# Kernel optimization log

Hardware: AMD Instinct MI355X
Metric: run time of the kernel (lower is better)

## Reference

```python
import jax, jax.numpy as jnp
import numpy as np

B, T, S = 32, 200, 256          # batch, decoder steps, encoder (memory) length
L = 512                          # latent_dims
U = 2 * L                        # LSTM units / attention units / attention_layer_size
E = 512                          # encoder memory feature dim
M = 80                           # mel_bins


def setup_inputs() -> dict:
    key = jax.random.key(0)
    ks = jax.random.split(key, 16)
    s = 0.05
    inputs = jax.random.normal(ks[0], (B, T, M), jnp.float32)
    memory = jax.random.normal(ks[1], (B, S, E), jnp.float32)
    # pre-net: Dense(2L, relu) -> Dropout -> Dense(L, relu) -> Dropout
    W1 = jax.random.normal(ks[2], (M, 2 * L), jnp.float32) * s
    b1 = jnp.zeros((2 * L,), jnp.float32)
    W2 = jax.random.normal(ks[3], (2 * L, L), jnp.float32) * s
    b2 = jnp.zeros((L,), jnp.float32)
    # LSTMCell(2L): input = concat(prenet_out [L], attention [U=2L]) -> 3L
    Wx = jax.random.normal(ks[4], (3 * L, 4 * U), jnp.float32) * s
    Wh = jax.random.normal(ks[5], (U, 4 * U), jnp.float32) * s
    b_lstm = jnp.zeros((4 * U,), jnp.float32)
    # Bahdanau attention (units=U): memory_layer, query_layer (no bias), score vector v
    Wm = jax.random.normal(ks[6], (E, U), jnp.float32) * s
    Wq = jax.random.normal(ks[7], (U, U), jnp.float32) * s
    v_att = jax.random.normal(ks[8], (U,), jnp.float32) * s
    # attention_layer (Dense, no bias): concat(cell_output [U], context [E]) -> U
    Wa = jax.random.normal(ks[9], (U + E, U), jnp.float32) * s
    # output projection to mel bins
    Wp = jax.random.normal(ks[10], (U, M), jnp.float32) * s
    bp = jnp.zeros((M,), jnp.float32)
    return dict(inputs=inputs, memory=memory, W1=W1, b1=b1, W2=W2, b2=b2,
                Wx=Wx, Wh=Wh, b_lstm=b_lstm, Wm=Wm, Wq=Wq, v_att=v_att,
                Wa=Wa, Wp=Wp, bp=bp)


def reference(inputs, memory, W1, b1, W2, b2, Wx, Wh, b_lstm, Wm, Wq, v_att, Wa, Wp, bp):
    # pre-net (inference: dropout is identity)
    x = jax.nn.relu(inputs @ W1 + b1)
    x = jax.nn.relu(x @ W2 + b2)                       # [B,T,L]
    keys = memory @ Wm                                 # precomputed attention keys [B,S,U]

    def step(carry, xt):
        h, c, attn = carry
        cell_in = jnp.concatenate([xt, attn], axis=-1)  # [B, 3L]
        z = cell_in @ Wx + h @ Wh + b_lstm              # [B, 4U]
        i, f, g, o = jnp.split(z, 4, axis=-1)
        c_new = jax.nn.sigmoid(f) * c + jax.nn.sigmoid(i) * jnp.tanh(g)
        h_new = jax.nn.sigmoid(o) * jnp.tanh(c_new)
        # Bahdanau additive attention
        q = h_new @ Wq                                  # [B,U]
        score = jnp.einsum('u,bsu->bs', v_att, jnp.tanh(keys + q[:, None, :]))
        align = jax.nn.softmax(score, axis=-1)          # [B,S]
        ctx = jnp.einsum('bs,bse->be', align, memory)   # [B,E]
        attn_new = jnp.concatenate([h_new, ctx], axis=-1) @ Wa  # [B,U]
        return (h_new, c_new, attn_new), attn_new

    init = (jnp.zeros((B, U), x.dtype), jnp.zeros((B, U), x.dtype), jnp.zeros((B, U), x.dtype))
    xs = jnp.swapaxes(x, 0, 1)                          # [T,B,L]
    (h, c, attn), ys = jax.lax.scan(step, init, xs)
    outs = jnp.swapaxes(ys, 0, 1)                       # [B,T,U]
    mel = outs @ Wp + bp                                # [B,T,M]
    return (mel, h, c, attn)
```

## Files before the change

kernel.cpp:

```cpp
#include <hip/hip_runtime.h>


typedef unsigned short us16;
typedef unsigned int u32;
typedef unsigned long long u64;
typedef __attribute__((ext_vector_type(8))) short bf16x8;
typedef __attribute__((ext_vector_type(4))) float f32x4;

#define MFMA16 __builtin_amdgcn_mfma_f32_16x16x32_bf16
#define AGT __HIP_MEMORY_SCOPE_AGENT

__device__ __forceinline__ us16 f2bf(float f){
  u32 u = __builtin_bit_cast(u32, f);
  u += 0x7fffu + ((u >> 16) & 1u);
  return (us16)(u >> 16);
}
__device__ __forceinline__ float bf2f(us16 h){
  return __builtin_bit_cast(float, ((u32)h) << 16);
}
__device__ __forceinline__ float h2f(us16 u){
  _Float16 h = __builtin_bit_cast(_Float16, u); return (float)h;
}
__device__ __forceinline__ us16 f2h(float f){
  _Float16 h = (_Float16)f; return __builtin_bit_cast(us16, h);
}
__device__ __forceinline__ void split3(float v, us16& s0, us16& s1, us16& s2){
  s0 = f2bf(v); float r = v - bf2f(s0);
  s1 = f2bf(r); r -= bf2f(s1);
  s2 = f2bf(r);
}
__device__ __forceinline__ float tanh_fast(float x){
  float e = __expf(-2.f * fmaxf(x, -40.f));
  return (1.f - e) / (1.f + e);
}

__device__ __forceinline__ u32 aload32(const u32* p){
  return __hip_atomic_load(p, __ATOMIC_RELAXED, AGT);
}
__device__ __forceinline__ void astoref(float* p, float v){
  __hip_atomic_store(p, v, __ATOMIC_RELAXED, AGT);
}
__device__ __forceinline__ void aaddf(float* p, float v){
  __hip_atomic_fetch_add(p, v, __ATOMIC_RELAXED, AGT);
}
__device__ __forceinline__ bf16x8 pin_reg(bf16x8 v){
  f32x4 t = __builtin_bit_cast(f32x4, v);
  asm volatile("" : "+v"(t));
  return __builtin_bit_cast(bf16x8, t);
}
__device__ __forceinline__ void f32_frag3(const float* p, float rs,
                                          bf16x8& f0, bf16x8& f1, bf16x8& f2){
  float4 t0 = *(const float4*)p;
  float4 t1 = *(const float4*)(p + 4);
  float tf[8] = {t0.x, t0.y, t0.z, t0.w, t1.x, t1.y, t1.z, t1.w};
#pragma unroll
  for (int i = 0; i < 8; ++i){
    float v = tf[i] * rs;
    us16 s0, s1, s2; split3(v, s0, s1, s2);
    f0[i] = (short)s0; f1[i] = (short)s1; f2[i] = (short)s2;
  }
}

#define OFF_WTA    0ull
#define OFF_WQT    50331648ull
#define OFF_X2P    56623104ull
#define OFF_KEYH   76283904ull
#define OFF_KEYL   93061120ull
#define OFF_X1     76283904ull
#define OFF_HIST   109838336ull
#define OFF_HROLL  129597440ull
#define OFF_UCROLL 155942912ull
#define OFF_SROLL  169115648ull
#define OFF_QROLL  169141376ull
#define OFF_CBUF   195355776ull
#define OFF_WAPN   195486848ull
#define OFF_BPERM  195732608ull
#define OFF_BAR    195748992ull
#define TOTAL_WS   195750016ull

#define WTPL 8388608ull
#define WQPL 1048576ull
#define X2PL 3276800ull

__global__ void k_zero_init(float* hroll0, float* ucroll, float* sroll,
                            float* cbuf, u32* bar){
  u32 id = blockIdx.x * 256u + threadIdx.x;
  const u32 gs = 65536u;
  for (u32 i = id; i < 32768u;   i += gs) hroll0[i] = 0.f;
  for (u32 i = id; i < 3293184u; i += gs) ucroll[i] = 0.f;
  for (u32 i = id; i < 6432u;    i += gs) sroll[i]  = (i < 32u) ? 1.f : 0.f;
  for (u32 i = id; i < 32768u;   i += gs) cbuf[i]   = 0.f;
  for (u32 i = id; i < 256u;     i += gs) bar[i]    = 0u;
}

__global__ void k_bperm(const float* __restrict__ bl, float* __restrict__ bpm){
  int c = blockIdx.x * 256 + threadIdx.x;
  if (c < 4096) bpm[((c & 1023) << 2) | (c >> 10)] = bl[c];
}

__global__ void k_transp3(const float* __restrict__ src, us16* __restrict__ dst,
                          int srows, int scols, int ldd, long long pstride, int perm){
  __shared__ float tile[32][33];
  int bx = blockIdx.x * 32, by = blockIdx.y * 32;
  int tx = threadIdx.x & 31, ty = threadIdx.x >> 5;
#pragma unroll
  for (int i = 0; i < 4; ++i){
    int r = by + ty + i * 8, c = bx + tx;
    tile[ty + i * 8][tx] = (r < srows && c < scols) ? src[(size_t)r * scols + c] : 0.f;
  }
  __syncthreads();
#pragma unroll
  for (int i = 0; i < 4; ++i){
    int c = bx + ty + i * 8;
    int r = by + tx;
    if (c < scols && r < srows){
      int oc = perm ? (((c & 1023) << 2) | (c >> 10)) : c;
      float v = tile[tx][ty + i * 8];
      us16 s0, s1, s2; split3(v, s0, s1, s2);
      size_t base = (size_t)oc * ldd + r;
      dst[base] = s0; dst[(size_t)pstride + base] = s1; dst[2ull * pstride + base] = s2;
    }
  }
}

template<int NP, int AF, int BF>
__global__ void __launch_bounds__(256)
k_gemm3(const void* __restrict__ Ap, const void* __restrict__ Bp, void* __restrict__ outp,
        int M, int N, int K, int mode, const float* __restrict__ aux, int ldd){
  __shared__ us16 At[NP][128][72];
  __shared__ us16 Bt[NP][64][72];
  const int tid = threadIdx.x, wv = tid >> 6, lane = tid & 63;
  const int r0 = lane & 15, kg = lane >> 4;
  const int rb = blockIdx.x * 128, cb = blockIdx.y * 64;
  f32x4 acc[2][4];
#pragma unroll
  for (int a = 0; a < 2; ++a)
#pragma unroll
    for (int b = 0; b < 4; ++b) acc[a][b] = (f32x4){0.f, 0.f, 0.f, 0.f};

  const int nkt = (K + 63) >> 6;
  for (int kt = 0; kt < nkt; ++kt){
    const int kb = kt * 64;
    for (int e = tid; e < 8192; e += 256){
      int r = e >> 6, k = e & 63, ga = rb + r, gk = kb + k;
      bool ok = (ga < M) && (gk < K);
      if constexpr (AF){
        float v = ok ? ((const float*)Ap)[(size_t)ga * K + gk] : 0.f;
        us16 s0, s1, s2; split3(v, s0, s1, s2);
        At[0][r][k] = s0;
        if constexpr (NP == 3){ At[1][r][k] = s1; At[2][r][k] = s2; }
      } else {
        At[0][r][k] = ok ? ((const us16*)Ap)[(size_t)ga * K + gk] : (us16)0;
      }
    }
    for (int e = tid; e < 4096; e += 256){
      int kr = e >> 6, c = e & 63, gk = kb + kr, gc = cb + c;
      bool ok = (gk < K) && (gc < N);
      if constexpr (BF){
        float v = ok ? ((const float*)Bp)[(size_t)gk * N + gc] : 0.f;
        us16 s0, s1, s2; split3(v, s0, s1, s2);
        Bt[0][c][kr] = s0;
        if constexpr (NP == 3){ Bt[1][c][kr] = s1; Bt[2][c][kr] = s2; }
      } else {
        Bt[0][c][kr] = ok ? ((const us16*)Bp)[(size_t)gk * N + gc] : (us16)0;
      }
    }
    __syncthreads();
#pragma unroll
    for (int kk = 0; kk < 64; kk += 32){
      bf16x8 af[NP][2];
#pragma unroll
      for (int p = 0; p < NP; ++p){
        af[p][0] = *(const bf16x8*)&At[p][wv * 32 + r0][kk + kg * 8];
        af[p][1] = *(const bf16x8*)&At[p][wv * 32 + 16 + r0][kk + kg * 8];
      }
#pragma unroll
      for (int cf = 0; cf < 4; ++cf){
        bf16x8 bv[NP];
#pragma unroll
        for (int p = 0; p < NP; ++p) bv[p] = *(const bf16x8*)&Bt[p][cf * 16 + r0][kk + kg * 8];
#pragma unroll
        for (int rf = 0; rf < 2; ++rf){
          acc[rf][cf] = MFMA16(af[0][rf], bv[0], acc[rf][cf], 0, 0, 0);
          if constexpr (NP == 3){
            acc[rf][cf] = MFMA16(af[0][rf], bv[1], acc[rf][cf], 0, 0, 0);
            acc[rf][cf] = MFMA16(af[1][rf], bv[0], acc[rf][cf], 0, 0, 0);
            acc[rf][cf] = MFMA16(af[0][rf], bv[2], acc[rf][cf], 0, 0, 0);
            acc[rf][cf] = MFMA16(af[1][rf], bv[1], acc[rf][cf], 0, 0, 0);
            acc[rf][cf] = MFMA16(af[2][rf], bv[0], acc[rf][cf], 0, 0, 0);
          }
        }
      }
    }
    __syncthreads();
  }
  us16* o16 = (us16*)outp; float* of = (float*)outp;
#pragma unroll
  for (int rf = 0; rf < 2; ++rf)
#pragma unroll
    for (int cf = 0; cf < 4; ++cf)
#pragma unroll
      for (int i = 0; i < 4; ++i){
        int r = rb + wv * 32 + rf * 16 + kg * 4 + i;
        int c = cb + cf * 16 + r0;
        if (r >= M || c >= N) continue;
        float v = acc[rf][cf][i];
        if (mode == 0){
          of[(size_t)r * ldd + c] = fmaxf(v + aux[c], 0.f);
        } else if (mode == 1){
          v = fmaxf(v + aux[c], 0.f);
          us16 s0, s1, s2; split3(v, s0, s1, s2);
          size_t b2 = (size_t)r * ldd + c;
          o16[b2] = s0; o16[X2PL + b2] = s1; o16[2 * X2PL + b2] = s2;
        } else if (mode == 2){
          us16 hh = f2h(v); float rem = v - h2f(hh); us16 hl = f2h(rem);
          size_t b2 = (size_t)r * 1024 + c;
          o16[b2] = hh; o16[WTPL + b2] = hl;
        } else if (mode == 3){
          float w = v + (r < 1024 ? aux[(size_t)r * 4096 + c] : 0.f);
          int pc = (c & 1023) * 4 + (c >> 10);
          us16 s0, s1, s2; split3(w, s0, s1, s2);
          size_t b2 = (size_t)pc * 2048 + 512 + r;
          o16[b2] = s0; o16[WTPL + b2] = s1; o16[2 * WTPL + b2] = s2;
        } else if (mode == 4){
          o16[(size_t)r * ldd + c] = f2bf(v);
        } else if (mode == 5){
          of[((size_t)(r & 31) * 200 + (r >> 5)) * 80 + c] = v + aux[c];
        } else {
          of[(size_t)r * ldd + c] = v;
        }
      }
}

__device__ __forceinline__ void gbar(u32* bar, u32 ep, int tid, int blk){
  __syncthreads();
  if (tid == 0){
    asm volatile("s_waitcnt vmcnt(0)" ::: "memory");
    u32 g = (u32)(blk >> 5);
    u32 old = __hip_atomic_fetch_add(&bar[g * 32], 1u, __ATOMIC_RELAXED, AGT);
    if (old == 32u * ep - 1u){
      u32 r = __hip_atomic_fetch_add(&bar[248], 1u, __ATOMIC_RELAXED, AGT);
      if (r == 8u * ep - 1u)
        __hip_atomic_store(&bar[252], ep, __ATOMIC_RELAXED, AGT);
    }
    while (aload32(&bar[252]) < ep) __builtin_amdgcn_s_sleep(1);
    __builtin_amdgcn_sched_barrier(0);
  }
  __syncthreads();
}

struct CoopA {
  const us16 *wta, *wqt, *x2p, *kh, *kl;
  const float *mem, *vatt, *bperm;
  us16 *hist;
  float *hroll, *ucroll, *sroll, *qroll, *cbuf;
  u32 *bar;
};

__global__ void __launch_bounds__(512, 2) k_coop(CoopA a){
  __shared__ us16 khi[32][1024];
  __shared__ us16 klo[32][1024];
  __shared__ float zp[8][512];
  __shared__ float esc[32];
  __shared__ float rs_lds[32];

  __builtin_amdgcn_fence(__ATOMIC_ACQUIRE, "agent");

  const int tid = threadIdx.x, blk = blockIdx.x;
  const int wv = tid >> 6, lane = tid & 63;
  const int r0 = lane & 15, kg = lane >> 4;
  const int cb_b = blk >> 3, cb_s0 = (blk & 7) * 32;
  const int colbase = blk * 16;
  const int u0 = lane * 16;

  bf16x8 wr[8][3];
#pragma unroll
  for (int ks = 0; ks < 8; ++ks){
    const size_t wb = (size_t)(colbase + r0) * 2048 + (size_t)wv * 256 + ks * 32 + kg * 8;
#pragma unroll
    for (int p = 0; p < 3; ++p)
      wr[ks][p] = pin_reg(*(const bf16x8*)&a.wta[(size_t)p * WTPL + wb]);
  }
  bf16x8 wq[4][3];
  if (blk < 64){
#pragma unroll
    for (int ks = 0; ks < 4; ++ks){
      const size_t wb = (size_t)(colbase + r0) * 1024 + (size_t)wv * 128 + ks * 32 + kg * 8;
#pragma unroll
      for (int p = 0; p < 3; ++p)
        wq[ks][p] = pin_reg(*(const bf16x8*)&a.wqt[(size_t)p * WQPL + wb]);
    }
  }

  {
    const size_t kbase = ((size_t)(cb_b * 256 + cb_s0)) * 1024;
    for (int i = tid; i < 4096; i += 512){
      int r = i >> 7, c8 = (i & 127) * 8;
      *(bf16x8*)&khi[r][c8] = *(const bf16x8*)&a.kh[kbase + (size_t)r * 1024 + c8];
      *(bf16x8*)&klo[r][c8] = *(const bf16x8*)&a.kl[kbase + (size_t)r * 1024 + c8];
    }
  }
  __syncthreads();

  u32 ep = 0;
  for (int t = 0; t < 200; ++t){
    {
      if (tid < 32) rs_lds[tid] = 1.f / a.sroll[(size_t)t * 32 + tid];
      __syncthreads();
      if (tid < 64){
        int flat = blk * 64 + tid;
        int b = flat >> 9, e = flat & 511;
        float v = a.ucroll[(size_t)t * 16384 + flat];
        a.hist[(size_t)(t * 32 + b) * 1536 + 1024 + e] = f2bf(v * rs_lds[b]);
      }
      f32x4 acc0 = (f32x4){0.f,0.f,0.f,0.f}, acc1 = acc0;
#pragma unroll
      for (int ks = 0; ks < 8; ++ks){
        const int k0 = wv * 256 + ks * 32;
        const int kf = k0 + kg * 8;
        bf16x8 w0 = wr[ks][0], w1 = wr[ks][1], w2 = wr[ks][2];
        bf16x8 a00, a01, a02, a10, a11, a12;
        if (wv < 2){
          const size_t xb0 = ((size_t)r0 * 200 + t) * 512 + kf;
          const size_t xb1 = ((size_t)(r0 + 16) * 200 + t) * 512 + kf;
          a00 = *(const bf16x8*)&a.x2p[xb0];
          a01 = *(const bf16x8*)&a.x2p[X2PL + xb0];
          a02 = *(const bf16x8*)&a.x2p[2 * X2PL + xb0];
          a10 = *(const bf16x8*)&a.x2p[xb1];
          a11 = *(const bf16x8*)&a.x2p[X2PL + xb1];
          a12 = *(const bf16x8*)&a.x2p[2 * X2PL + xb1];
        } else if (wv < 6){
          const int hk = kf - 512;
          const float* hp0 = a.hroll + (size_t)t * 32768 + (size_t)r0 * 1024 + hk;
          f32_frag3(hp0,         1.f, a00, a01, a02);
          f32_frag3(hp0 + 16384, 1.f, a10, a11, a12);
        } else {
          const int ek = kf - 1536;
          const float* up = a.ucroll + (size_t)t * 16384 + (size_t)r0 * 512 + ek;
          f32_frag3(up,        rs_lds[r0],      a00, a01, a02);
          f32_frag3(up + 8192, rs_lds[r0 + 16], a10, a11, a12);
        }
        acc0 = MFMA16(a00, w0, acc0, 0,0,0); acc0 = MFMA16(a00, w1, acc0, 0,0,0);
        acc0 = MFMA16(a01, w0, acc0, 0,0,0); acc0 = MFMA16(a00, w2, acc0, 0,0,0);
        acc0 = MFMA16(a01, w1, acc0, 0,0,0); acc0 = MFMA16(a02, w0, acc0, 0,0,0);
        acc1 = MFMA16(a10, w0, acc1, 0,0,0); acc1 = MFMA16(a10, w1, acc1, 0,0,0);
        acc1 = MFMA16(a11, w0, acc1, 0,0,0); acc1 = MFMA16(a10, w2, acc1, 0,0,0);
        acc1 = MFMA16(a11, w1, acc1, 0,0,0); acc1 = MFMA16(a12, w0, acc1, 0,0,0);
      }
#pragma unroll
      for (int i = 0; i < 4; ++i){
        zp[wv][(kg * 4 + i) * 16 + r0]      = acc0[i];
        zp[wv][(16 + kg * 4 + i) * 16 + r0] = acc1[i];
      }
      __syncthreads();
      float z = 0.f;
#pragma unroll
      for (int w = 0; w < 8; ++w) z += zp[w][tid];
      z += a.bperm[colbase + (tid & 15)];
      __syncthreads();
      zp[0][tid] = z;
      __syncthreads();
      if (tid < 128){
        int b = tid >> 2, ul = tid & 3, u = blk * 4 + ul;
        float zi = zp[0][b * 16 + ul * 4 + 0];
        float zf = zp[0][b * 16 + ul * 4 + 1];
        float zg = zp[0][b * 16 + ul * 4 + 2];
        float zo = zp[0][b * 16 + ul * 4 + 3];
        float co = a.cbuf[b * 1024 + u];
        float cn = (1.f / (1.f + expf(-zf))) * co + (1.f / (1.f + expf(-zi))) * tanhf(zg);
        float hn = (1.f / (1.f + expf(-zo))) * tanhf(cn);
        a.cbuf[b * 1024 + u] = cn;
        astoref(&a.hroll[(size_t)(t + 1) * 32768 + b * 1024 + u], hn);
        us16 s0, s1, s2; split3(hn, s0, s1, s2);
        a.hist[((size_t)(t + 1) * 32 + b) * 1536 + u] = s0;
      }
    }
    gbar(a.bar, ++ep, tid, blk);

    if (blk < 64){
      f32x4 acc0 = (f32x4){0.f,0.f,0.f,0.f}, acc1 = acc0;
#pragma unroll
      for (int ks = 0; ks < 4; ++ks){
        const int kf = wv * 128 + ks * 32 + kg * 8;
        bf16x8 w0 = wq[ks][0], w1 = wq[ks][1], w2 = wq[ks][2];
        bf16x8 a00, a01, a02, a10, a11, a12;
        const float* hp0 = a.hroll + (size_t)(t + 1) * 32768 + (size_t)r0 * 1024 + kf;
        f32_frag3(hp0,         1.f, a00, a01, a02);
        f32_frag3(hp0 + 16384, 1.f, a10, a11, a12);
        acc0 = MFMA16(a00, w0, acc0, 0,0,0); acc0 = MFMA16(a00, w1, acc0, 0,0,0);
        acc0 = MFMA16(a01, w0, acc0, 0,0,0); acc0 = MFMA16(a00, w2, acc0, 0,0,0);
        acc0 = MFMA16(a01, w1, acc0, 0,0,0); acc0 = MFMA16(a02, w0, acc0, 0,0,0);
        acc1 = MFMA16(a10, w0, acc1, 0,0,0); acc1 = MFMA16(a10, w1, acc1, 0,0,0);
        acc1 = MFMA16(a11, w0, acc1, 0,0,0); acc1 = MFMA16(a10, w2, acc1, 0,0,0);
        acc1 = MFMA16(a11, w1, acc1, 0,0,0); acc1 = MFMA16(a12, w0, acc1, 0,0,0);
      }
#pragma unroll
      for (int i = 0; i < 4; ++i){
        zp[wv][(kg * 4 + i) * 16 + r0]      = acc0[i];
        zp[wv][(16 + kg * 4 + i) * 16 + r0] = acc1[i];
      }
      __syncthreads();
      float q = 0.f;
#pragma unroll
      for (int w = 0; w < 8; ++w) q += zp[w][tid];
      astoref(&a.qroll[(size_t)t * 32768 + (size_t)(tid >> 4) * 1024 + colbase + (tid & 15)], q);
    }
    gbar(a.bar, ++ep, tid, blk);

    {
      float qv[16], vv[16];
      {
        const float* qp = a.qroll + (size_t)t * 32768 + (size_t)cb_b * 1024 + u0;
        float4 q0 = *(const float4*)qp;
        float4 q1 = *(const float4*)(qp + 4);
        float4 q2 = *(const float4*)(qp + 8);
        float4 q3 = *(const float4*)(qp + 12);
        qv[0]=q0.x; qv[1]=q0.y; qv[2]=q0.z; qv[3]=q0.w;
        qv[4]=q1.x; qv[5]=q1.y; qv[6]=q1.z; qv[7]=q1.w;
        qv[8]=q2.x; qv[9]=q2.y; qv[10]=q2.z; qv[11]=q2.w;
        qv[12]=q3.x; qv[13]=q3.y; qv[14]=q3.z; qv[15]=q3.w;
        float4 v0 = *(const float4*)(a.vatt + u0);
        float4 v1 = *(const float4*)(a.vatt + u0 + 4);
        float4 v2 = *(const float4*)(a.vatt + u0 + 8);
        float4 v3 = *(const float4*)(a.vatt + u0 + 12);
        vv[0]=v0.x; vv[1]=v0.y; vv[2]=v0.z; vv[3]=v0.w;
        vv[4]=v1.x; vv[5]=v1.y; vv[6]=v1.z; vv[7]=v1.w;
        vv[8]=v2.x; vv[9]=v2.y; vv[10]=v2.z; vv[11]=v2.w;
        vv[12]=v3.x; vv[13]=v3.y; vv[14]=v3.z; vv[15]=v3.w;
      }
#pragma unroll
      for (int m = 0; m < 4; ++m){
        const int sl = wv * 4 + m;
        bf16x8 h0 = *(const bf16x8*)&khi[sl][u0];
        bf16x8 h1 = *(const bf16x8*)&khi[sl][u0 + 8];
        bf16x8 l0 = *(const bf16x8*)&klo[sl][u0];
        bf16x8 l1 = *(const bf16x8*)&klo[sl][u0 + 8];
        float part = 0.f;
#pragma unroll
        for (int j = 0; j < 8; ++j){
          float kva = h2f((us16)h0[j]) + h2f((us16)l0[j]);
          part += vv[j] * tanh_fast(kva + qv[j]);
          float kvb = h2f((us16)h1[j]) + h2f((us16)l1[j]);
          part += vv[8 + j] * tanh_fast(kvb + qv[8 + j]);
        }
#pragma unroll
        for (int off = 32; off; off >>= 1) part += __shfl_xor(part, off);
        if (lane == 0) esc[sl] = __expf(part);
      }
      __syncthreads();
      if (tid == 0){
        float bs = 0.f;
#pragma unroll
        for (int i = 0; i < 32; ++i) bs += esc[i];
        aaddf(&a.sroll[(size_t)(t + 1) * 32 + cb_b], bs);
      }
      {
        float ac0 = 0.f, ac1 = 0.f, ac2 = 0.f, ac3 = 0.f;
        const float* mrow = a.mem + ((size_t)(cb_b * 256 + cb_s0)) * 512 + tid;
#pragma unroll
        for (int j = 0; j < 32; j += 4){
          ac0 += esc[j]     * mrow[(size_t)j * 512];
          ac1 += esc[j + 1] * mrow[(size_t)(j + 1) * 512];
          ac2 += esc[j + 2] * mrow[(size_t)(j + 2) * 512];
          ac3 += esc[j + 3] * mrow[(size_t)(j + 3) * 512];
        }
        aaddf(&a.ucroll[(size_t)(t + 1) * 16384 + cb_b * 512 + tid], (ac0 + ac1) + (ac2 + ac3));
      }
    }
    gbar(a.bar, ++ep, tid, blk);
  }

  {
    if (tid < 32) rs_lds[tid] = 1.f / a.sroll[(size_t)200 * 32 + tid];
    __syncthreads();
    if (tid < 64){
      int flat = blk * 64 + tid;
      int b = flat >> 9, e = flat & 511;
      float v = a.ucroll[(size_t)200 * 16384 + flat];
      a.hist[(size_t)(200 * 32 + b) * 1536 + 1024 + e] = f2bf(v * rs_lds[b]);
    }
  }
}

__global__ void k_copy_hc(const float* __restrict__ h, const float* __restrict__ c,
                          float* __restrict__ out){
  int i = blockIdx.x * 256 + threadIdx.x;
  if (i < 32768){
    out[512000 + i] = h[i];
    out[544768 + i] = c[i];
  }
}

extern "C" void kernel_launch(void* const* d_in, const int* in_sizes, int n_in,
                              void* d_out, int out_size, void* d_ws, size_t ws_size,
                              hipStream_t stream){
  const float* inputs = (const float*)d_in[0];
  const float* memory = (const float*)d_in[1];
  const float* W1     = (const float*)d_in[2];
  const float* b1     = (const float*)d_in[3];
  const float* W2     = (const float*)d_in[4];
  const float* b2     = (const float*)d_in[5];
  const float* Wx     = (const float*)d_in[6];
  const float* Wh     = (const float*)d_in[7];
  const float* b_lstm = (const float*)d_in[8];
  const float* Wm     = (const float*)d_in[9];
  const float* Wq     = (const float*)d_in[10];
  const float* v_att  = (const float*)d_in[11];
  const float* Wa     = (const float*)d_in[12];
  const float* Wp     = (const float*)d_in[13];
  const float* bp     = (const float*)d_in[14];
  float* out = (float*)d_out;
  char* ws = (char*)d_ws;
  if (ws_size < TOTAL_WS) return;

  us16* WTA    = (us16*)(ws + OFF_WTA);
  us16* WQT    = (us16*)(ws + OFF_WQT);
  us16* X2P    = (us16*)(ws + OFF_X2P);
  us16* KEYH   = (us16*)(ws + OFF_KEYH);
  float* X1    = (float*)(ws + OFF_X1);
  us16* HIST   = (us16*)(ws + OFF_HIST);
  float* HROLL = (float*)(ws + OFF_HROLL);
  float* UCROLL= (float*)(ws + OFF_UCROLL);
  float* SROLL = (float*)(ws + OFF_SROLL);
  float* QROLL = (float*)(ws + OFF_QROLL);
  float* CBUF  = (float*)(ws + OFF_CBUF);
  us16* WAPN   = (us16*)(ws + OFF_WAPN);
  float* BPM   = (float*)(ws + OFF_BPERM);
  u32*  BAR    = (u32*)(ws + OFF_BAR);

  k_zero_init<<<256, 256, 0, stream>>>(HROLL, UCROLL, SROLL, CBUF, BAR);
  k_bperm<<<16, 256, 0, stream>>>(b_lstm, BPM);
  k_transp3<<<dim3(32, 32), 256, 0, stream>>>(Wq, WQT, 1024, 1024, 1024, (long long)WQPL, 0);
  k_transp3<<<dim3(128, 16), 256, 0, stream>>>(Wx, WTA, 512, 4096, 2048, (long long)WTPL, 1);

  k_gemm3<3,1,1><<<dim3(12, 64), 256, 0, stream>>>(Wa, Wx + (size_t)512 * 4096, WTA,
                                                   1536, 4096, 1024, 3, Wh, 0);
  k_gemm3<3,1,1><<<dim3(12, 2), 256, 0, stream>>>(Wa, Wp, WAPN, 1536, 80, 1024, 4, nullptr, 80);
  k_gemm3<3,1,1><<<dim3(50, 16), 256, 0, stream>>>(inputs, W1, X1, 6400, 1024, 80, 0, b1, 1024);
  k_gemm3<3,1,1><<<dim3(50, 8), 256, 0, stream>>>(X1, W2, X2P, 6400, 512, 1024, 1, b2, 512);
  k_gemm3<3,1,1><<<dim3(64, 16), 256, 0, stream>>>(memory, Wm, KEYH, 8192, 1024, 512, 2, nullptr, 1024);

  CoopA ca;
  ca.wta = WTA; ca.wqt = WQT; ca.x2p = X2P; ca.kh = KEYH; ca.kl = KEYH + WTPL;
  ca.mem = memory; ca.vatt = v_att; ca.bperm = BPM;
  ca.hist = HIST; ca.hroll = HROLL; ca.ucroll = UCROLL; ca.sroll = SROLL;
  ca.qroll = QROLL; ca.cbuf = CBUF; ca.bar = BAR;
  void* args[] = {(void*)&ca};
  hipLaunchCooperativeKernel((const void*)k_coop, dim3(256), dim3(512), args, 0, stream);

  k_gemm3<1,0,0><<<dim3(50, 2), 256, 0, stream>>>(HIST + (size_t)32 * 1536, WAPN, out,
                                                  6400, 80, 1536, 5, bp, 0);
  k_gemm3<1,0,1><<<dim3(1, 16), 256, 0, stream>>>(HIST + (size_t)200 * 32 * 1536, Wa,
                                                  out + 577536, 32, 1024, 1536, 6, nullptr, 1024);
  k_copy_hc<<<128, 256, 0, stream>>>(HROLL + (size_t)200 * 32768, CBUF, out);
}
```

Before: 12.45 ms.

## Hoist input-projection GEMM out of recurrence and defer history conversion

The prenet-output contribution to the LSTM gates (x_t @ Wx) is now computed for all timesteps in one large GEMM before the cooperative kernel, and the recurrent step reads the precomputed gate partials instead of running MFMA on them. Waves 0-1 of each block, now freed, prefetch the next step's gate partials and memory rows. Writing the bf16 history moves out of the loop into a separate k_hist kernel. Other changes: a single q buffer replaces the per-step q roll, the Wq fragments are reloaded each step rather than held in registers, the gate nonlinearities use fast exp-based sigmoid and tanh, and launch bounds change to one block per CU. The goal is to shorten the serial per-step critical path, at the cost of a larger workspace and extra global traffic.

```diff
diff --git a/kernel.cpp b/kernel.cpp
--- a/kernel.cpp
+++ b/kernel.cpp
@@ -33,15 +33,27 @@
   float e = __expf(-2.f * fmaxf(x, -40.f));
   return (1.f - e) / (1.f + e);
 }
+__device__ __forceinline__ float sigf(float x){
+  return 1.f / (1.f + __expf(-x));
+}
 
 __device__ __forceinline__ u32 aload32(const u32* p){
   return __hip_atomic_load(p, __ATOMIC_RELAXED, AGT);
 }
+__device__ __forceinline__ u64 aload64(const u64* p){
+  return __hip_atomic_load(p, __ATOMIC_RELAXED, AGT);
+}
 __device__ __forceinline__ void astoref(float* p, float v){
   __hip_atomic_store(p, v, __ATOMIC_RELAXED, AGT);
 }
 __device__ __forceinline__ void aaddf(float* p, float v){
   __hip_atomic_fetch_add(p, v, __ATOMIC_RELAXED, AGT);
+}
+__device__ __forceinline__ float4 aloadf4(const float* p){
+  union { u64 u[2]; float4 f; } t;
+  const u64* q = (const u64*)p;
+  t.u[0] = aload64(q); t.u[1] = aload64(q + 1);
+  return t.f;
 }
 __device__ __forceinline__ bf16x8 pin_reg(bf16x8 v){
   f32x4 t = __builtin_bit_cast(f32x4, v);
@@ -63,34 +75,33 @@
 
 #define OFF_WTA    0ull
 #define OFF_WQT    50331648ull
-#define OFF_X2P    56623104ull
-#define OFF_KEYH   76283904ull
-#define OFF_KEYL   93061120ull
-#define OFF_X1     76283904ull
-#define OFF_HIST   109838336ull
-#define OFF_HROLL  129597440ull
-#define OFF_UCROLL 155942912ull
-#define OFF_SROLL  169115648ull
-#define OFF_QROLL  169141376ull
-#define OFF_CBUF   195355776ull
-#define OFF_WAPN   195486848ull
-#define OFF_BPERM  195732608ull
-#define OFF_BAR    195748992ull
-#define TOTAL_WS   195750016ull
+#define OFF_X2F    56623104ull
+#define OFF_KEYH   69730304ull
+#define OFF_KEYL   86507520ull
+#define OFF_X1     69730304ull
+#define OFF_HIST   103284736ull
+#define OFF_HROLL  123043840ull
+#define OFF_UCR    149389312ull
+#define OFF_SR     162562048ull
+#define OFF_QB     162587776ull
+#define OFF_CB     162718848ull
+#define OFF_WAPN   162849920ull
+#define OFF_BPERM  163095680ull
+#define OFF_BAR    163112064ull
+#define OFF_ZX     163113088ull
+#define TOTAL_WS   267970688ull
 
 #define WTPL 8388608ull
 #define WQPL 1048576ull
-#define X2PL 3276800ull
-
-__global__ void k_zero_init(float* hroll0, float* ucroll, float* sroll,
-                            float* cbuf, u32* bar){
+
+__global__ void k_zero_init(float* hroll0, float* ucr, float* sr, float* cbuf, u32* bar){
   u32 id = blockIdx.x * 256u + threadIdx.x;
   const u32 gs = 65536u;
   for (u32 i = id; i < 32768u;   i += gs) hroll0[i] = 0.f;
-  for (u32 i = id; i < 3293184u; i += gs) ucroll[i] = 0.f;
-  for (u32 i = id; i < 6432u;    i += gs) sroll[i]  = (i < 32u) ? 1.f : 0.f;
-  for (u32 i = id; i < 32768u;   i += gs) cbuf[i]   = 0.f;
-  for (u32 i = id; i < 256u;     i += gs) bar[i]    = 0u;
+  for (u32 i = id; i < 3293184u; i += gs) ucr[i]  = 0.f;
+  for (u32 i = id; i < 6432u;    i += gs) sr[i]   = (i < 32u) ? 1.f : 0.f;
+  for (u32 i = id; i < 32768u;   i += gs) cbuf[i] = 0.f;
+  for (u32 i = id; i < 256u;     i += gs) bar[i]  = 0u;
 }
 
 __global__ void k_bperm(const float* __restrict__ bl, float* __restrict__ bpm){
@@ -207,11 +218,6 @@
         float v = acc[rf][cf][i];
         if (mode == 0){
           of[(size_t)r * ldd + c] = fmaxf(v + aux[c], 0.f);
-        } else if (mode == 1){
-          v = fmaxf(v + aux[c], 0.f);
-          us16 s0, s1, s2; split3(v, s0, s1, s2);
-          size_t b2 = (size_t)r * ldd + c;
-          o16[b2] = s0; o16[X2PL + b2] = s1; o16[2 * X2PL + b2] = s2;
         } else if (mode == 2){
           us16 hh = f2h(v); float rem = v - h2f(hh); us16 hl = f2h(rem);
           size_t b2 = (size_t)r * 1024 + c;
@@ -226,6 +232,9 @@
           o16[(size_t)r * ldd + c] = f2bf(v);
         } else if (mode == 5){
           of[((size_t)(r & 31) * 200 + (r >> 5)) * 80 + c] = v + aux[c];
+        } else if (mode == 7){
+          int pc = (c & 1023) * 4 + (c >> 10);
+          of[((size_t)(r % 200) * 32 + (r / 200)) * 4096 + pc] = v;
         } else {
           of[(size_t)r * ldd + c] = v;
         }
@@ -250,14 +259,13 @@
 }
 
 struct CoopA {
-  const us16 *wta, *wqt, *x2p, *kh, *kl;
-  const float *mem, *vatt, *bperm;
-  us16 *hist;
-  float *hroll, *ucroll, *sroll, *qroll, *cbuf;
+  const us16 *wta, *wqt, *kh, *kl;
+  const float *mem, *vatt, *bperm, *zx;
+  float *hroll, *ucr, *sr, *qb, *cbuf;
   u32 *bar;
 };
 
-__global__ void __launch_bounds__(512, 2) k_coop(CoopA a){
+__global__ void __launch_bounds__(512, 1) k_coop(CoopA a){
   __shared__ us16 khi[32][1024];
   __shared__ us16 klo[32][1024];
   __shared__ float zp[8][512];
@@ -274,21 +282,14 @@
   const int u0 = lane * 16;
 
   bf16x8 wr[8][3];
-#pragma unroll
-  for (int ks = 0; ks < 8; ++ks){
-    const size_t wb = (size_t)(colbase + r0) * 2048 + (size_t)wv * 256 + ks * 32 + kg * 8;
-#pragma unroll
-    for (int p = 0; p < 3; ++p)
-      wr[ks][p] = pin_reg(*(const bf16x8*)&a.wta[(size_t)p * WTPL + wb]);
-  }
-  bf16x8 wq[4][3];
-  if (blk < 64){
-#pragma unroll
-    for (int ks = 0; ks < 4; ++ks){
-      const size_t wb = (size_t)(colbase + r0) * 1024 + (size_t)wv * 128 + ks * 32 + kg * 8;
+  if (wv >= 2){
+#pragma unroll
+    for (int ks = 0; ks < 8; ++ks){
+      const size_t wb = (size_t)(colbase + r0) * 2048 + 512 +
+                        (size_t)(wv - 2) * 256 + ks * 32 + kg * 8;
 #pragma unroll
       for (int p = 0; p < 3; ++p)
-        wq[ks][p] = pin_reg(*(const bf16x8*)&a.wqt[(size_t)p * WQPL + wb]);
+        wr[ks][p] = pin_reg(*(const bf16x8*)&a.wta[(size_t)p * WTPL + wb]);
     }
   }
 
@@ -305,57 +306,50 @@
   u32 ep = 0;
   for (int t = 0; t < 200; ++t){
     {
-      if (tid < 32) rs_lds[tid] = 1.f / a.sroll[(size_t)t * 32 + tid];
+      if (tid < 32) rs_lds[tid] = 1.f / a.sr[(size_t)t * 32 + tid];
       __syncthreads();
-      if (tid < 64){
-        int flat = blk * 64 + tid;
-        int b = flat >> 9, e = flat & 511;
-        float v = a.ucroll[(size_t)t * 16384 + flat];
-        a.hist[(size_t)(t * 32 + b) * 1536 + 1024 + e] = f2bf(v * rs_lds[b]);
-      }
-      f32x4 acc0 = (f32x4){0.f,0.f,0.f,0.f}, acc1 = acc0;
-#pragma unroll
-      for (int ks = 0; ks < 8; ++ks){
-        const int k0 = wv * 256 + ks * 32;
-        const int kf = k0 + kg * 8;
-        bf16x8 w0 = wr[ks][0], w1 = wr[ks][1], w2 = wr[ks][2];
-        bf16x8 a00, a01, a02, a10, a11, a12;
-        if (wv < 2){
-          const size_t xb0 = ((size_t)r0 * 200 + t) * 512 + kf;
-          const size_t xb1 = ((size_t)(r0 + 16) * 200 + t) * 512 + kf;
-          a00 = *(const bf16x8*)&a.x2p[xb0];
-          a01 = *(const bf16x8*)&a.x2p[X2PL + xb0];
-          a02 = *(const bf16x8*)&a.x2p[2 * X2PL + xb0];
-          a10 = *(const bf16x8*)&a.x2p[xb1];
-          a11 = *(const bf16x8*)&a.x2p[X2PL + xb1];
-          a12 = *(const bf16x8*)&a.x2p[2 * X2PL + xb1];
-        } else if (wv < 6){
-          const int hk = kf - 512;
-          const float* hp0 = a.hroll + (size_t)t * 32768 + (size_t)r0 * 1024 + hk;
-          f32_frag3(hp0,         1.f, a00, a01, a02);
-          f32_frag3(hp0 + 16384, 1.f, a10, a11, a12);
-        } else {
-          const int ek = kf - 1536;
-          const float* up = a.ucroll + (size_t)t * 16384 + (size_t)r0 * 512 + ek;
-          f32_frag3(up,        rs_lds[r0],      a00, a01, a02);
-          f32_frag3(up + 8192, rs_lds[r0 + 16], a10, a11, a12);
+      if (wv < 2){
+        const float* mslice = a.mem + ((size_t)(cb_b * 256 + cb_s0)) * 512;
+        float s = mslice[tid * 128] + mslice[tid * 128 + 32] +
+                  mslice[tid * 128 + 64] + mslice[tid * 128 + 96];
+        if (t < 199)
+          s += a.zx[((size_t)(t + 1) * 32 + (tid & 31)) * 4096 + colbase];
+        asm volatile("" :: "v"(s));
+      } else {
+        f32x4 acc0 = (f32x4){0.f,0.f,0.f,0.f}, acc1 = acc0;
+#pragma unroll
+        for (int ks = 0; ks < 8; ++ks){
+          const int kl2 = (wv - 2) * 256 + ks * 32 + kg * 8;
+          bf16x8 w0 = wr[ks][0], w1 = wr[ks][1], w2 = wr[ks][2];
+          bf16x8 a00, a01, a02, a10, a11, a12;
+          if (wv < 6){
+            const float* hp0 = a.hroll + (size_t)t * 32768 + (size_t)r0 * 1024 + kl2;
+            f32_frag3(hp0,         1.f, a00, a01, a02);
+            f32_frag3(hp0 + 16384, 1.f, a10, a11, a12);
+          } else {
+            const int ek = kl2 - 1024;
+            const float* up = a.ucr + (size_t)t * 16384 + (size_t)r0 * 512 + ek;
+            f32_frag3(up,        rs_lds[r0],      a00, a01, a02);
+            f32_frag3(up + 8192, rs_lds[r0 + 16], a10, a11, a12);
+          }
+          acc0 = MFMA16(a00, w0, acc0, 0,0,0); acc0 = MFMA16(a00, w1, acc0, 0,0,0);
+          acc0 = MFMA16(a01, w0, acc0, 0,0,0); acc0 = MFMA16(a00, w2, acc0, 0,0,0);
+          acc0 = MFMA16(a01, w1, acc0, 0,0,0); acc0 = MFMA16(a02, w0, acc0, 0,0,0);
+          acc1 = MFMA16(a10, w0, acc1, 0,0,0); acc1 = MFMA16(a10, w1, acc1, 0,0,0);
+          acc1 = MFMA16(a11, w0, acc1, 0,0,0); acc1 = MFMA16(a10, w2, acc1, 0,0,0);
+          acc1 = MFMA16(a11, w1, acc1, 0,0,0); acc1 = MFMA16(a12, w0, acc1, 0,0,0);
         }
-        acc0 = MFMA16(a00, w0, acc0, 0,0,0); acc0 = MFMA16(a00, w1, acc0, 0,0,0);
-        acc0 = MFMA16(a01, w0, acc0, 0,0,0); acc0 = MFMA16(a00, w2, acc0, 0,0,0);
-        acc0 = MFMA16(a01, w1, acc0, 0,0,0); acc0 = MFMA16(a02, w0, acc0, 0,0,0);
-        acc1 = MFMA16(a10, w0, acc1, 0,0,0); acc1 = MFMA16(a10, w1, acc1, 0,0,0);
-        acc1 = MFMA16(a11, w0, acc1, 0,0,0); acc1 = MFMA16(a10, w2, acc1, 0,0,0);
-        acc1 = MFMA16(a11, w1, acc1, 0,0,0); acc1 = MFMA16(a12, w0, acc1, 0,0,0);
-      }
-#pragma unroll
-      for (int i = 0; i < 4; ++i){
-        zp[wv][(kg * 4 + i) * 16 + r0]      = acc0[i];
-        zp[wv][(16 + kg * 4 + i) * 16 + r0] = acc1[i];
+#pragma unroll
+        for (int i = 0; i < 4; ++i){
+          zp[wv][(kg * 4 + i) * 16 + r0]      = acc0[i];
+          zp[wv][(16 + kg * 4 + i) * 16 + r0] = acc1[i];
+        }
       }
       __syncthreads();
       float z = 0.f;
 #pragma unroll
-      for (int w = 0; w < 8; ++w) z += zp[w][tid];
+      for (int w = 2; w < 8; ++w) z += zp[w][tid];
+      z += a.zx[((size_t)t * 32 + (tid >> 4)) * 4096 + colbase + (tid & 15)];
       z += a.bperm[colbase + (tid & 15)];
       __syncthreads();
       zp[0][tid] = z;
@@ -367,12 +361,10 @@
         float zg = zp[0][b * 16 + ul * 4 + 2];
         float zo = zp[0][b * 16 + ul * 4 + 3];
         float co = a.cbuf[b * 1024 + u];
-        float cn = (1.f / (1.f + expf(-zf))) * co + (1.f / (1.f + expf(-zi))) * tanhf(zg);
-        float hn = (1.f / (1.f + expf(-zo))) * tanhf(cn);
+        float cn = sigf(zf) * co + sigf(zi) * tanh_fast(zg);
+        float hn = sigf(zo) * tanh_fast(cn);
         a.cbuf[b * 1024 + u] = cn;
         astoref(&a.hroll[(size_t)(t + 1) * 32768 + b * 1024 + u], hn);
-        us16 s0, s1, s2; split3(hn, s0, s1, s2);
-        a.hist[((size_t)(t + 1) * 32 + b) * 1536 + u] = s0;
       }
     }
     gbar(a.bar, ++ep, tid, blk);
@@ -382,7 +374,10 @@
 #pragma unroll
       for (int ks = 0; ks < 4; ++ks){
         const int kf = wv * 128 + ks * 32 + kg * 8;
-        bf16x8 w0 = wq[ks][0], w1 = wq[ks][1], w2 = wq[ks][2];
+        const size_t wb = (size_t)(colbase + r0) * 1024 + kf;
+        bf16x8 w0 = *(const bf16x8*)&a.wqt[wb];
+        bf16x8 w1 = *(const bf16x8*)&a.wqt[WQPL + wb];
+        bf16x8 w2 = *(const bf16x8*)&a.wqt[2 * WQPL + wb];
         bf16x8 a00, a01, a02, a10, a11, a12;
         const float* hp0 = a.hroll + (size_t)(t + 1) * 32768 + (size_t)r0 * 1024 + kf;
         f32_frag3(hp0,         1.f, a00, a01, a02);
@@ -403,18 +398,16 @@
       float q = 0.f;
 #pragma unroll
       for (int w = 0; w < 8; ++w) q += zp[w][tid];
-      astoref(&a.qroll[(size_t)t * 32768 + (size_t)(tid >> 4) * 1024 + colbase + (tid & 15)], q);
+      astoref(&a.qb[(size_t)(tid >> 4) * 1024 + colbase + (tid & 15)], q);
     }
     gbar(a.bar, ++ep, tid, blk);
 
     {
       float qv[16], vv[16];
       {
-        const float* qp = a.qroll + (size_t)t * 32768 + (size_t)cb_b * 1024 + u0;
-        float4 q0 = *(const float4*)qp;
-        float4 q1 = *(const float4*)(qp + 4);
-        float4 q2 = *(const float4*)(qp + 8);
-        float4 q3 = *(const float4*)(qp + 12);
+        const float* qp = a.qb + (size_t)cb_b * 1024 + u0;
+        float4 q0 = aloadf4(qp), q1 = aloadf4(qp + 4);
+        float4 q2 = aloadf4(qp + 8), q3 = aloadf4(qp + 12);
         qv[0]=q0.x; qv[1]=q0.y; qv[2]=q0.z; qv[3]=q0.w;
         qv[4]=q1.x; qv[5]=q1.y; qv[6]=q1.z; qv[7]=q1.w;
         qv[8]=q2.x; qv[9]=q2.y; qv[10]=q2.z; qv[11]=q2.w;
@@ -452,7 +445,7 @@
         float bs = 0.f;
 #pragma unroll
         for (int i = 0; i < 32; ++i) bs += esc[i];
-        aaddf(&a.sroll[(size_t)(t + 1) * 32 + cb_b], bs);
+        aaddf(&a.sr[(size_t)(t + 1) * 32 + cb_b], bs);
       }
       {
         float ac0 = 0.f, ac1 = 0.f, ac2 = 0.f, ac3 = 0.f;
@@ -464,21 +457,23 @@
           ac2 += esc[j + 2] * mrow[(size_t)(j + 2) * 512];
           ac3 += esc[j + 3] * mrow[(size_t)(j + 3) * 512];
         }
-        aaddf(&a.ucroll[(size_t)(t + 1) * 16384 + cb_b * 512 + tid], (ac0 + ac1) + (ac2 + ac3));
+        aaddf(&a.ucr[(size_t)(t + 1) * 16384 + cb_b * 512 + tid], (ac0 + ac1) + (ac2 + ac3));
       }
     }
     gbar(a.bar, ++ep, tid, blk);
   }
-
-  {
-    if (tid < 32) rs_lds[tid] = 1.f / a.sroll[(size_t)200 * 32 + tid];
-    __syncthreads();
-    if (tid < 64){
-      int flat = blk * 64 + tid;
-      int b = flat >> 9, e = flat & 511;
-      float v = a.ucroll[(size_t)200 * 16384 + flat];
-      a.hist[(size_t)(200 * 32 + b) * 1536 + 1024 + e] = f2bf(v * rs_lds[b]);
-    }
+}
+
+__global__ void k_hist(const float* __restrict__ hroll, const float* __restrict__ ucr,
+                       const float* __restrict__ sr, us16* __restrict__ hist){
+  int row = blockIdx.x;
+  int t = row >> 5, b = row & 31;
+  float rs = 1.f / sr[(size_t)t * 32 + b];
+  for (int c = threadIdx.x; c < 1536; c += 256){
+    us16 v;
+    if (c < 1024) v = f2bf(hroll[(size_t)t * 32768 + b * 1024 + c]);
+    else          v = f2bf(ucr[(size_t)t * 16384 + b * 512 + (c - 1024)] * rs);
+    hist[(size_t)row * 1536 + c] = v;
   }
 }
 
@@ -515,42 +510,43 @@
 
   us16* WTA    = (us16*)(ws + OFF_WTA);
   us16* WQT    = (us16*)(ws + OFF_WQT);
-  us16* X2P    = (us16*)(ws + OFF_X2P);
+  float* X2F   = (float*)(ws + OFF_X2F);
   us16* KEYH   = (us16*)(ws + OFF_KEYH);
   float* X1    = (float*)(ws + OFF_X1);
   us16* HIST   = (us16*)(ws + OFF_HIST);
   float* HROLL = (float*)(ws + OFF_HROLL);
-  float* UCROLL= (float*)(ws + OFF_UCROLL);
-  float* SROLL = (float*)(ws + OFF_SROLL);
-  float* QROLL = (float*)(ws + OFF_QROLL);
-  float* CBUF  = (float*)(ws + OFF_CBUF);
+  float* UCR   = (float*)(ws + OFF_UCR);
+  float* SR    = (float*)(ws + OFF_SR);
+  float* QB    = (float*)(ws + OFF_QB);
+  float* CB    = (float*)(ws + OFF_CB);
   us16* WAPN   = (us16*)(ws + OFF_WAPN);
   float* BPM   = (float*)(ws + OFF_BPERM);
   u32*  BAR    = (u32*)(ws + OFF_BAR);
-
-  k_zero_init<<<256, 256, 0, stream>>>(HROLL, UCROLL, SROLL, CBUF, BAR);
+  float* ZX    = (float*)(ws + OFF_ZX);
+
+  k_zero_init<<<256, 256, 0, stream>>>(HROLL, UCR, SR, CB, BAR);
   k_bperm<<<16, 256, 0, stream>>>(b_lstm, BPM);
   k_transp3<<<dim3(32, 32), 256, 0, stream>>>(Wq, WQT, 1024, 1024, 1024, (long long)WQPL, 0);
-  k_transp3<<<dim3(128, 16), 256, 0, stream>>>(Wx, WTA, 512, 4096, 2048, (long long)WTPL, 1);
 
   k_gemm3<3,1,1><<<dim3(12, 64), 256, 0, stream>>>(Wa, Wx + (size_t)512 * 4096, WTA,
                                                    1536, 4096, 1024, 3, Wh, 0);
   k_gemm3<3,1,1><<<dim3(12, 2), 256, 0, stream>>>(Wa, Wp, WAPN, 1536, 80, 1024, 4, nullptr, 80);
   k_gemm3<3,1,1><<<dim3(50, 16), 256, 0, stream>>>(inputs, W1, X1, 6400, 1024, 80, 0, b1, 1024);
-  k_gemm3<3,1,1><<<dim3(50, 8), 256, 0, stream>>>(X1, W2, X2P, 6400, 512, 1024, 1, b2, 512);
+  k_gemm3<3,1,1><<<dim3(50, 8), 256, 0, stream>>>(X1, W2, X2F, 6400, 512, 1024, 0, b2, 512);
+  k_gemm3<3,1,1><<<dim3(50, 64), 256, 0, stream>>>(X2F, Wx, ZX, 6400, 4096, 512, 7, nullptr, 0);
   k_gemm3<3,1,1><<<dim3(64, 16), 256, 0, stream>>>(memory, Wm, KEYH, 8192, 1024, 512, 2, nullptr, 1024);
 
   CoopA ca;
-  ca.wta = WTA; ca.wqt = WQT; ca.x2p = X2P; ca.kh = KEYH; ca.kl = KEYH + WTPL;
-  ca.mem = memory; ca.vatt = v_att; ca.bperm = BPM;
-  ca.hist = HIST; ca.hroll = HROLL; ca.ucroll = UCROLL; ca.sroll = SROLL;
-  ca.qroll = QROLL; ca.cbuf = CBUF; ca.bar = BAR;
+  ca.wta = WTA; ca.wqt = WQT; ca.kh = KEYH; ca.kl = KEYH + WTPL;
+  ca.mem = memory; ca.vatt = v_att; ca.bperm = BPM; ca.zx = ZX;
+  ca.hroll = HROLL; ca.ucr = UCR; ca.sr = SR; ca.qb = QB; ca.cbuf = CB; ca.bar = BAR;
   void* args[] = {(void*)&ca};
   hipLaunchCooperativeKernel((const void*)k_coop, dim3(256), dim3(512), args, 0, stream);
 
+  k_hist<<<6432, 256, 0, stream>>>(HROLL, UCR, SR, HIST);
   k_gemm3<1,0,0><<<dim3(50, 2), 256, 0, stream>>>(HIST + (size_t)32 * 1536, WAPN, out,
                                                   6400, 80, 1536, 5, bp, 0);
   k_gemm3<1,0,1><<<dim3(1, 16), 256, 0, stream>>>(HIST + (size_t)200 * 32 * 1536, Wa,
                                                   out + 577536, 32, 1024, 1536, 6, nullptr, 1024);
-  k_copy_hc<<<128, 256, 0, stream>>>(HROLL + (size_t)200 * 32768, CBUF, out);
-}
+  k_copy_hc<<<128, 256, 0, stream>>>(HROLL + (size_t)200 * 32768, CB, out);
+}
```

New measurement: 14.31 ms. 1.15x slower.
